# Optimization experiments

Measured on AMD Instinct MI355X. Metric: run time of the kernel, lower is better.

The kernel has to match this reference:

```python
import jax, jax.numpy as jnp
import numpy as np

B, T, V, E, H = 64, 512, 8192, 1024, 2048


def setup_inputs() -> dict:
    key = jax.random.key(0)
    k = jax.random.split(key, 8)
    idx = jax.random.randint(k[0], (B, T), 0, V)
    targets = jax.random.randint(k[1], (B, T), 0, V)
    s = 0.02
    W_E = jax.random.normal(k[2], (V, E), jnp.float32) * s
    start = jnp.zeros((1, H), jnp.float32)
    W_xh = jax.random.normal(k[3], (E + H, H), jnp.float32) * s  # Linear(E+H -> H)
    b_xh = jnp.zeros((H,), jnp.float32)
    W_head = jax.random.normal(k[4], (H, V), jnp.float32) * s
    b_head = jnp.zeros((V,), jnp.float32)
    return {"idx": idx, "targets": targets, "W_E": W_E, "start": start,
            "W_xh": W_xh, "b_xh": b_xh, "W_head": W_head, "b_head": b_head}


def reference(idx, targets, W_E, start, W_xh, b_xh, W_head, b_head):
    b, t = idx.shape
    emb = W_E[idx]  # [B, T, E]
    # split concat-linear: cat([x,h]) @ W_xh == x @ Wx + h @ Wh (same math)
    Wx, Wh = W_xh[:E], W_xh[E:]
    xproj = jnp.einsum('bte,eh->bth', emb, Wx) + b_xh  # precompute input part

    def step(h_prev, xp_t):
        h_t = jnp.tanh(xp_t + h_prev @ Wh)
        return h_t, h_t

    h0 = jnp.broadcast_to(start, (b, H))
    _, hs = jax.lax.scan(step, h0, jnp.swapaxes(xproj, 0, 1))  # [T, B, H]
    hidden = jnp.swapaxes(hs, 0, 1)  # [B, T, H]
    logits = jnp.einsum('bth,hv->btv', hidden, W_head) + b_head

    # cross entropy with ignore_index=-1
    logp = jax.nn.log_softmax(logits, axis=-1)
    mask = targets != -1
    tsafe = jnp.where(mask, targets, 0)
    nll = -jnp.take_along_axis(logp, tsafe[..., None], axis=-1)[..., 0]
    loss = jnp.sum(nll * mask) / jnp.maximum(jnp.sum(mask), 1)
    return logits, loss
```

## Files before the change

### kernel.cpp

```cpp
#include <hip/hip_runtime.h>
#include <hip/hip_bf16.h>
#include <math.h>
#include <stdint.h>

#define Bb 64
#define Tt 512
#define Vv 8192
#define Ee 1024
#define Hh 2048

typedef unsigned short u16;
typedef unsigned long long u64;
typedef __attribute__((ext_vector_type(8))) short bf16x8;
typedef __attribute__((ext_vector_type(8))) _Float16 f16x8;
typedef __attribute__((ext_vector_type(4))) float f32x4;

__device__ __forceinline__ u16 f2b(float f) {
  unsigned u = __float_as_uint(f);
  u += 0x7FFF + ((u >> 16) & 1);
  return (u16)(u >> 16);
}
__device__ __forceinline__ float b2f(u16 h) {
  return __uint_as_float(((unsigned)h) << 16);
}
__device__ __forceinline__ u16 f2h_bits(float f) {
  union { _Float16 h; u16 u; } c;
  c.h = (_Float16)f;
  return c.u;
}
__device__ __forceinline__ u64 pack4(u16 a, u16 b, u16 c, u16 d) {
  return (u64)a | ((u64)b << 16) | ((u64)c << 32) | ((u64)d << 48);
}

__device__ __forceinline__ void gload16f(f16x8& dst, const void* addr) {
  asm volatile("global_load_dwordx4 %0, %1, off sc1"
               : "=v"(dst) : "v"(addr) : "memory");
}

__device__ __forceinline__ void gll16(const u16* g, u16* l) {
  __builtin_amdgcn_global_load_lds((__attribute__((address_space(1))) void*)g,
                                   (__attribute__((address_space(3))) void*)l, 16, 0, 0);
}

__device__ __forceinline__ float wave_max(float v) {
  #pragma unroll
  for (int d = 32; d; d >>= 1) v = fmaxf(v, __shfl_xor(v, d, 64));
  return v;
}
__device__ __forceinline__ float wave_sum(float v) {
  #pragma unroll
  for (int d = 32; d; d >>= 1) v += __shfl_xor(v, d, 64);
  return v;
}


__global__ __launch_bounds__(256)
void embed_cast(const float* __restrict__ WE, const int* __restrict__ idx,
                u16* __restrict__ emb2) {
  const int m = blockIdx.x;
  const int row = idx[m];
  const float4 v = ((const float4*)(WE + (size_t)row * Ee))[threadIdx.x];
  ushort4 hi, lo;
  hi.x = f2b(v.x); lo.x = f2b(v.x - b2f(hi.x));
  hi.y = f2b(v.y); lo.y = f2b(v.y - b2f(hi.y));
  hi.z = f2b(v.z); lo.z = f2b(v.z - b2f(hi.z));
  hi.w = f2b(v.w); lo.w = f2b(v.w - b2f(hi.w));
  u16* d = emb2 + (size_t)m * 2048;
  ((ushort4*)d)[threadIdx.x] = hi;
  ((ushort4*)(d + Ee))[threadIdx.x] = lo;
}

__global__ __launch_bounds__(256)
void transpose_cast(const float* __restrict__ src, u16* __restrict__ dst,
                    int R, int C, int dup) {
  __shared__ float tile[32][33];
  const int bi = blockIdx.x;
  const int bj = blockIdx.y;
  const int tid = threadIdx.x;
  const int r  = tid >> 3;
  const int c4 = (tid & 7) * 4;
  float4 v = *(const float4*)(src + (size_t)(bj * 32 + r) * C + bi * 32 + c4);
  tile[r][c4 + 0] = v.x; tile[r][c4 + 1] = v.y;
  tile[r][c4 + 2] = v.z; tile[r][c4 + 3] = v.w;
  __syncthreads();
  const int RL = R << dup;
  ushort4 o;
  o.x = f2b(tile[c4 + 0][r]); o.y = f2b(tile[c4 + 1][r]);
  o.z = f2b(tile[c4 + 2][r]); o.w = f2b(tile[c4 + 3][r]);
  u16* d = dst + (size_t)(bi * 32 + r) * RL + bj * 32 + c4;
  *(ushort4*)d = o;
  if (dup) *(ushort4*)(d + R) = o;
}

__global__ __launch_bounds__(256)
void transpose_cast_f16(const float* __restrict__ src, u16* __restrict__ dst,
                        int R, int C) {
  __shared__ float tile[32][33];
  const int bi = blockIdx.x;
  const int bj = blockIdx.y;
  const int tid = threadIdx.x;
  const int r  = tid >> 3;
  const int c4 = (tid & 7) * 4;
  float4 v = *(const float4*)(src + (size_t)(bj * 32 + r) * C + bi * 32 + c4);
  tile[r][c4 + 0] = v.x; tile[r][c4 + 1] = v.y;
  tile[r][c4 + 2] = v.z; tile[r][c4 + 3] = v.w;
  __syncthreads();
  ushort4 o;
  o.x = f2h_bits(tile[c4 + 0][r]); o.y = f2h_bits(tile[c4 + 1][r]);
  o.z = f2h_bits(tile[c4 + 2][r]); o.w = f2h_bits(tile[c4 + 3][r]);
  *(ushort4*)(dst + (size_t)(bi * 32 + r) * R + bj * 32 + c4) = o;
}

__global__ __launch_bounds__(256)
void h0_init(const float* __restrict__ start, u16* __restrict__ hbuf) {
  const int b = blockIdx.x;
  #pragma unroll
  for (int j = 0; j < 8; ++j) {
    int n = threadIdx.x * 8 + j;
    hbuf[(size_t)b * 2048 + n] = f2h_bits(start[n]);
  }
}

template <int MODE>
__global__ __launch_bounds__(256, 2)
void gemm_bt(const u16* __restrict__ A, const u16* __restrict__ Bt,
             const float* __restrict__ bias, void* __restrict__ outp,
             float* __restrict__ pm, float* __restrict__ ps,
             int M, int N, int K) {
  __shared__ u16 ldsA[128 * 32];
  __shared__ u16 ldsB[128 * 32];
  __shared__ float sm_[2][2][64];
  __shared__ float ss_[2][2][64];
  const int tid = threadIdx.x;
  const int lane = tid & 63;
  const int w = tid >> 6;
  const int wr = w >> 1, wc = w & 1;

  const int nwg = gridDim.x * gridDim.y;
  const int lin = blockIdx.y * gridDim.x + blockIdx.x;
  const int swz = (lin & 7) * (nwg >> 3) + (lin >> 3);
  const int bm = swz % gridDim.x;
  const int bn = swz / gridDim.x;

  const int srow = w * 32 + (lane >> 2);
  const int scol = (lane & 3) * 8;
  const u16* a0 = A + (size_t)(bm * 128 + srow) * K + scol;
  const u16* b0 = Bt + (size_t)(bn * 128 + srow) * K + scol;
  u16* lA0 = ldsA + w * 1024;
  u16* lA1 = ldsA + w * 1024 + 512;
  u16* lB0 = ldsB + w * 1024;
  u16* lB1 = ldsB + w * 1024 + 512;

  f32x4 acc[4][4];
  #pragma unroll
  for (int m = 0; m < 4; ++m)
    #pragma unroll
    for (int n = 0; n < 4; ++n)
      acc[m][n] = (f32x4){0.f, 0.f, 0.f, 0.f};

  const int nk = K >> 5;
  for (int kt = 0; kt < nk; ++kt) {
    __syncthreads();
    const u16* ak = a0 + kt * 32;
    const u16* bk = b0 + kt * 32;
    gll16(ak, lA0);
    gll16(ak + 16 * (size_t)K, lA1);
    gll16(bk, lB0);
    gll16(bk + 16 * (size_t)K, lB1);
    __syncthreads();
    bf16x8 af[4], bfr[4];
    #pragma unroll
    for (int i = 0; i < 4; ++i) {
      af[i]  = *(const bf16x8*)&ldsA[(wr * 64 + i * 16 + (lane & 15)) * 32 + (lane >> 4) * 8];
      bfr[i] = *(const bf16x8*)&ldsB[(wc * 64 + i * 16 + (lane & 15)) * 32 + (lane >> 4) * 8];
    }
    #pragma unroll
    for (int m = 0; m < 4; ++m)
      #pragma unroll
      for (int n = 0; n < 4; ++n)
        acc[m][n] = __builtin_amdgcn_mfma_f32_16x16x32_bf16(af[m], bfr[n], acc[m][n], 0, 0, 0);
  }

  const int r0 = bm * 128 + wr * 64 + (lane >> 4) * 4;
  const int c0 = bn * 128 + wc * 64 + (lane & 15);

  if (MODE == 0) {
    float bv[4];
    #pragma unroll
    for (int n = 0; n < 4; ++n) bv[n] = bias[c0 + n * 16];
    #pragma unroll
    for (int m = 0; m < 4; ++m) {
      #pragma unroll
      for (int q = 0; q < 4; ++q) {
        const int row = r0 + m * 16 + q;
        float v[4];
        float mx = -1e30f;
        #pragma unroll
        for (int n = 0; n < 4; ++n) {
          v[n] = acc[m][n][q] + bv[n];
          ((float*)outp)[(size_t)row * N + c0 + n * 16] = v[n];
          mx = fmaxf(mx, v[n]);
        }
        #pragma unroll
        for (int d = 1; d < 16; d <<= 1) mx = fmaxf(mx, __shfl_xor(mx, d, 64));
        float se = 0.f;
        #pragma unroll
        for (int n = 0; n < 4; ++n) se += expf(v[n] - mx);
        #pragma unroll
        for (int d = 1; d < 16; d <<= 1) se += __shfl_xor(se, d, 64);
        if ((lane & 15) == 0) {
          const int rl = m * 16 + (lane >> 4) * 4 + q;
          sm_[wc][wr][rl] = mx;
          ss_[wc][wr][rl] = se;
        }
      }
    }
    __syncthreads();
    if (w < 2) {
      float m0 = sm_[0][w][lane], m1 = sm_[1][w][lane];
      float s0 = ss_[0][w][lane], s1 = ss_[1][w][lane];
      float Mx = fmaxf(m0, m1);
      float S = s0 * expf(m0 - Mx) + s1 * expf(m1 - Mx);
      const int row = bm * 128 + w * 64 + lane;
      pm[(size_t)row * 64 + bn] = Mx;
      ps[(size_t)row * 64 + bn] = S;
    }
  } else {
    #pragma unroll
    for (int n = 0; n < 4; ++n) {
      const int col = c0 + n * 16;
      const float bv = bias[col];
      #pragma unroll
      for (int m = 0; m < 4; ++m) {
        #pragma unroll
        for (int q = 0; q < 4; ++q) {
          const int row = r0 + m * 16 + q;
          float v = acc[m][n][q] + bv;
          const int b = row >> 9, t = row & 511;
          ((u16*)outp)[((size_t)t * Bb + b) * N + col] = f2b(v);
        }
      }
    }
  }
}

__global__ __launch_bounds__(512, 2)
void rnn_scan(const u16* __restrict__ WhT, const u16* __restrict__ xp,
              u16* __restrict__ hbuf, u16* __restrict__ hidden,
              unsigned* __restrict__ sync) {
  __shared__ u16 whi[65536];
  __shared__ float red[4096];

  const int bid = blockIdx.x;
  const int g = bid >> 6;
  const int colg = bid & 63;
  const int rowbase = g * 16;
  const int col0 = colg * 32;
  const int tid = threadIdx.x;
  const int lane = tid & 63;
  const int w = tid >> 6;

  for (int i = tid; i < 8192; i += 512) {
    const int ch = i & 3;
    const int cl = (i >> 2) & 15;
    const int kt = (i >> 6) & 63;
    const int c2 = (i >> 12) & 1;
    bf16x8 v = *(const bf16x8*)(WhT + (size_t)(col0 + c2 * 16 + cl) * 2048 + kt * 32 + ch * 8);
    *(bf16x8*)&whi[(size_t)(c2 * 64 + kt) * 512 + ch * 128 + cl * 8] = v;
  }
  __syncthreads();

  unsigned* cnt = sync + g * 64;
  bool dead = false;

  const int hrow = rowbase + (lane & 15);

  ushort4 xv = {0, 0, 0, 0};
  if (w < 2)
    xv = *(const ushort4*)(xp + (size_t)hrow * 2048 + col0 + w * 16 + (lane >> 4) * 4);

  for (int t = 0; t < Tt; ++t) {
    const u16* hp = hbuf + (size_t)(t & 1) * (64 * 2048);
    u16*       hn = hbuf + (size_t)((t + 1) & 1) * (64 * 2048);

    f16x8 qh[8];
    const u16* hb = hp + (size_t)hrow * 2048 + (lane >> 4) * 8;
    #pragma unroll
    for (int kt = 0; kt < 8; ++kt)
      gload16f(qh[kt], hb + (w * 8 + kt) * 32);
    asm volatile("s_waitcnt vmcnt(0)" ::: "memory");
    __builtin_amdgcn_sched_barrier(0);

    f32x4 a0 = (f32x4){0.f, 0.f, 0.f, 0.f};
    f32x4 a1 = (f32x4){0.f, 0.f, 0.f, 0.f};
    #pragma unroll
    for (int kt = 0; kt < 8; ++kt) {
      const int ktG = w * 8 + kt;
      f16x8 w0 = *(const f16x8*)&whi[(size_t)(0 * 64 + ktG) * 512 + (lane >> 4) * 128 + (lane & 15) * 8];
      f16x8 w1 = *(const f16x8*)&whi[(size_t)(1 * 64 + ktG) * 512 + (lane >> 4) * 128 + (lane & 15) * 8];
      a0 = __builtin_amdgcn_mfma_f32_16x16x32_f16(w0, qh[kt], a0, 0, 0, 0);
      a1 = __builtin_amdgcn_mfma_f32_16x16x32_f16(w1, qh[kt], a1, 0, 0, 0);
    }

    *(f32x4*)&red[(w) * 256 + lane * 4]     = a0;
    *(f32x4*)&red[(8 + w) * 256 + lane * 4] = a1;
    __syncthreads();

    if (w < 2) {
      f32x4 ac = (f32x4){0.f, 0.f, 0.f, 0.f};
      #pragma unroll
      for (int j = 0; j < 8; ++j)
        ac += *(const f32x4*)&red[(w * 8 + j) * 256 + lane * 4];
      const int cl0 = (lane >> 4) * 4;
      u16 hf[4], hbv[4];
      #pragma unroll
      for (int qq = 0; qq < 4; ++qq) {
        float v = tanhf(ac[qq] + b2f(((const u16*)&xv)[qq]));
        hf[qq]  = f2h_bits(v);
        hbv[qq] = f2b(v);
      }
      u64 ph = pack4(hf[0], hf[1], hf[2], hf[3]);
      u64 pb = pack4(hbv[0], hbv[1], hbv[2], hbv[3]);
      u16* hd = hn + (size_t)hrow * 2048 + col0 + w * 16 + cl0;
      __hip_atomic_store((u64*)hd, ph, __ATOMIC_RELAXED, __HIP_MEMORY_SCOPE_AGENT);
      *(u64*)(hidden + ((size_t)hrow * Tt + t) * Hh + col0 + w * 16 + cl0) = pb;
    }

    __syncthreads();
    if (w < 2 && t + 1 < Tt)
      xv = *(const ushort4*)(xp + ((size_t)(t + 1) * Bb + hrow) * 2048 + col0 + w * 16 + (lane >> 4) * 4);
    if (tid == 0) {
      unsigned old = __hip_atomic_fetch_add(cnt, 1u, __ATOMIC_RELAXED, __HIP_MEMORY_SCOPE_AGENT);
      if (old != (unsigned)(t * 64 + 63) && !dead) {
        unsigned polls = 0;
        while (__hip_atomic_load(cnt, __ATOMIC_RELAXED, __HIP_MEMORY_SCOPE_AGENT)
               < (unsigned)((t + 1) * 64)) {
          if (++polls > 4000000u) { dead = true; break; }
        }
      }
    }
    __syncthreads();
  }
}


__global__ __launch_bounds__(256)
void nll_from_partials(const float* __restrict__ pm, const float* __restrict__ ps,
                       const float* __restrict__ logits, const int* __restrict__ tgt,
                       float* __restrict__ nll) {
  const int r = blockIdx.x * 4 + (threadIdx.x >> 6);
  const int lane = threadIdx.x & 63;
  float m = pm[(size_t)r * 64 + lane];
  float s = ps[(size_t)r * 64 + lane];
  float M = wave_max(m);
  float S = wave_sum(s * expf(m - M));
  if (lane == 0) {
    const int tg = tgt[r];
    float o = 0.f;
    if (tg != -1) o = M + logf(S) - logits[(size_t)r * Vv + tg];
    nll[r] = o;
  }
}

__global__ __launch_bounds__(256)
void loss_reduce(const float* __restrict__ nll, const int* __restrict__ tgt,
                 float* __restrict__ out) {
  const int tid = threadIdx.x;
  float s = 0.f, c = 0.f;
  for (int i = tid; i < Bb * Tt; i += 256) {
    s += nll[i];
    c += (tgt[i] != -1) ? 1.f : 0.f;
  }
  s = wave_sum(s);
  c = wave_sum(c);
  __shared__ float as_[4], ac_[4];
  const int w = tid >> 6;
  if ((tid & 63) == 0) { as_[w] = s; ac_[w] = c; }
  __syncthreads();
  if (tid == 0) {
    float S = as_[0] + as_[1] + as_[2] + as_[3];
    float C = ac_[0] + ac_[1] + ac_[2] + ac_[3];
    out[0] = S / fmaxf(C, 1.f);
  }
}


extern "C" void kernel_launch(void* const* d_in, const int* in_sizes, int n_in,
                              void* d_out, int out_size, void* d_ws, size_t ws_size,
                              hipStream_t stream) {
  const int*   idx    = (const int*)d_in[0];
  const int*   tgt    = (const int*)d_in[1];
  const float* W_E    = (const float*)d_in[2];
  const float* start  = (const float*)d_in[3];
  const float* W_xh   = (const float*)d_in[4];
  const float* b_xh   = (const float*)d_in[5];
  const float* W_head = (const float*)d_in[6];
  const float* b_head = (const float*)d_in[7];

  char* ws = (char*)d_ws;
  u16*      emb2   = (u16*)(ws);
  u16*      hidden = (u16*)(ws);
  u16*      xproj  = (u16*)(ws + (size_t)128 * 1024 * 1024);
  float*    pm     = (float*)(ws + (size_t)128 * 1024 * 1024);
  float*    ps     = (float*)(ws + (size_t)136 * 1024 * 1024);
  u16*      WheadT = (u16*)(ws + (size_t)256 * 1024 * 1024);
  u16*      WhT    = (u16*)(ws + (size_t)288 * 1024 * 1024);
  u16*      WxT2   = (u16*)(ws + (size_t)304 * 1024 * 1024);
  u16*      hbuf   = (u16*)(ws + (size_t)312 * 1024 * 1024);
  float*    nll    = (float*)(ws + (size_t)313 * 1024 * 1024);
  unsigned* sync   = (unsigned*)(ws + (size_t)313 * 1024 * 1024 + 128 * 1024);

  embed_cast<<<Bb * Tt, 256, 0, stream>>>(W_E, idx, emb2);
  transpose_cast<<<dim3(Hh / 32, Ee / 32), 256, 0, stream>>>(W_xh, WxT2, Ee, Hh, 1);
  transpose_cast_f16<<<dim3(Hh / 32, Hh / 32), 256, 0, stream>>>(W_xh + (size_t)Ee * Hh, WhT, Hh, Hh);
  transpose_cast<<<dim3(Vv / 32, Hh / 32), 256, 0, stream>>>(W_head, WheadT, Hh, Vv, 0);
  h0_init<<<Bb, 256, 0, stream>>>(start, hbuf);
  hipMemsetAsync(sync, 0, 1024, stream);

  gemm_bt<1><<<dim3(256, 16), 256, 0, stream>>>(emb2, WxT2, b_xh, xproj, nullptr, nullptr,
                                                Bb * Tt, Hh, 2048);

  rnn_scan<<<256, 512, 0, stream>>>(WhT, xproj, hbuf, hidden, sync);

  gemm_bt<0><<<dim3(256, 64), 256, 0, stream>>>(hidden, WheadT, b_head, d_out, pm, ps,
                                                Bb * Tt, Vv, 2048);

  nll_from_partials<<<Bb * Tt / 4, 256, 0, stream>>>(pm, ps, (const float*)d_out, tgt, nll);
  loss_reduce<<<1, 256, 0, stream>>>(nll, tgt, (float*)d_out + ((size_t)out_size - 1));
}
```

Baseline: 4.554 ms.

## Replace 128x128 GEMM with double-buffered 256x256 tile GEMM using swizzled LDS

Replaces the simple 128x128 tile GEMM, which synchronised on every K=32 step, with a 512-thread 256x256 tile kernel. It uses K=64 steps, double-buffered LDS staging interleaved with MFMA phases, an XOR-swizzled LDS layout to avoid bank conflicts, and s_setprio around the MFMA bursts. Both the input projection and the head projection now use it, and the softmax partials shrink from 64 to 32 per row, so the NLL kernel is updated to match. The aim is to hide global-load latency and raise data reuse per tile. In exchange it uses 128KB of LDS with one block per CU and needs a larger register footprint.

```diff
diff --git a/kernel.cpp b/kernel.cpp
--- a/kernel.cpp
+++ b/kernel.cpp
@@ -37,7 +37,7 @@
                : "=v"(dst) : "v"(addr) : "memory");
 }
 
-__device__ __forceinline__ void gll16(const u16* g, u16* l) {
+__device__ __forceinline__ void gll16(const u16* g, const u16* l) {
   __builtin_amdgcn_global_load_lds((__attribute__((address_space(1))) void*)g,
                                    (__attribute__((address_space(3))) void*)l, 16, 0, 0);
 }
@@ -121,124 +121,175 @@
   }
 }
 
+#define A0BASE 0
+#define A1BASE 16384
+#define B0BASE 32768
+#define B1BASE 49152
+#define MM(a, b, c) __builtin_amdgcn_mfma_f32_16x16x32_bf16(a, b, c, 0, 0, 0)
+
+#define DSA(AB, MH, KS, I) \
+  (*(const bf16x8*)&lds[(AB) + (wm * 128 + ((MH) * 4 + (I)) * 16 + l15) * 64 + (((KS) * 32 + l16 * 8) ^ axr)])
+#define DSB(BB, KS, J) \
+  (*(const bf16x8*)&lds[(BB) + (wn * 64 + (J) * 16 + l15) * 64 + (((KS) * 32 + l16 * 8) ^ axr)])
+
+#define PHASE(ABUF, BBUF, MH, KS, RB, STG)                                   \
+  {                                                                          \
+    bf16x8 a0_ = DSA(ABUF, MH, KS, 0), a1_ = DSA(ABUF, MH, KS, 1),           \
+           a2_ = DSA(ABUF, MH, KS, 2), a3_ = DSA(ABUF, MH, KS, 3);           \
+    if (RB) {                                                                \
+      b0_ = DSB(BBUF, KS, 0); b1_ = DSB(BBUF, KS, 1);                        \
+      b2_ = DSB(BBUF, KS, 2); b3_ = DSB(BBUF, KS, 3);                        \
+    }                                                                        \
+    STG;                                                                     \
+    asm volatile("s_waitcnt vmcnt(4)" ::: "memory");                         \
+    __builtin_amdgcn_s_barrier();                                            \
+    asm volatile("s_waitcnt lgkmcnt(0)" ::: "memory");                       \
+    __builtin_amdgcn_sched_barrier(0);                                       \
+    __builtin_amdgcn_s_setprio(1);                                           \
+    acc[(MH)*4+0][0] = MM(a0_, b0_, acc[(MH)*4+0][0]);                       \
+    acc[(MH)*4+0][1] = MM(a0_, b1_, acc[(MH)*4+0][1]);                       \
+    acc[(MH)*4+0][2] = MM(a0_, b2_, acc[(MH)*4+0][2]);                       \
+    acc[(MH)*4+0][3] = MM(a0_, b3_, acc[(MH)*4+0][3]);                       \
+    acc[(MH)*4+1][0] = MM(a1_, b0_, acc[(MH)*4+1][0]);                       \
+    acc[(MH)*4+1][1] = MM(a1_, b1_, acc[(MH)*4+1][1]);                       \
+    acc[(MH)*4+1][2] = MM(a1_, b2_, acc[(MH)*4+1][2]);                       \
+    acc[(MH)*4+1][3] = MM(a1_, b3_, acc[(MH)*4+1][3]);                       \
+    acc[(MH)*4+2][0] = MM(a2_, b0_, acc[(MH)*4+2][0]);                       \
+    acc[(MH)*4+2][1] = MM(a2_, b1_, acc[(MH)*4+2][1]);                       \
+    acc[(MH)*4+2][2] = MM(a2_, b2_, acc[(MH)*4+2][2]);                       \
+    acc[(MH)*4+2][3] = MM(a2_, b3_, acc[(MH)*4+2][3]);                       \
+    acc[(MH)*4+3][0] = MM(a3_, b0_, acc[(MH)*4+3][0]);                       \
+    acc[(MH)*4+3][1] = MM(a3_, b1_, acc[(MH)*4+3][1]);                       \
+    acc[(MH)*4+3][2] = MM(a3_, b2_, acc[(MH)*4+3][2]);                       \
+    acc[(MH)*4+3][3] = MM(a3_, b3_, acc[(MH)*4+3][3]);                       \
+    __builtin_amdgcn_s_setprio(0);                                           \
+    __builtin_amdgcn_s_barrier();                                            \
+  }
+
 template <int MODE>
-__global__ __launch_bounds__(256, 2)
-void gemm_bt(const u16* __restrict__ A, const u16* __restrict__ Bt,
+__global__ __launch_bounds__(512)
+void gemm256(const u16* __restrict__ A, const u16* __restrict__ Bt,
              const float* __restrict__ bias, void* __restrict__ outp,
              float* __restrict__ pm, float* __restrict__ ps,
              int M, int N, int K) {
-  __shared__ u16 ldsA[128 * 32];
-  __shared__ u16 ldsB[128 * 32];
-  __shared__ float sm_[2][2][64];
-  __shared__ float ss_[2][2][64];
+  __shared__ u16 lds[65536];
+
   const int tid = threadIdx.x;
   const int lane = tid & 63;
   const int w = tid >> 6;
-  const int wr = w >> 1, wc = w & 1;
+  const int wm = w >> 2;
+  const int wn = w & 3;
+  const int l15 = lane & 15, l16 = lane >> 4;
+  const int axr = (l15 & 7) << 3;
 
   const int nwg = gridDim.x * gridDim.y;
   const int lin = blockIdx.y * gridDim.x + blockIdx.x;
   const int swz = (lin & 7) * (nwg >> 3) + (lin >> 3);
   const int bm = swz % gridDim.x;
   const int bn = swz / gridDim.x;
-
-  const int srow = w * 32 + (lane >> 2);
-  const int scol = (lane & 3) * 8;
-  const u16* a0 = A + (size_t)(bm * 128 + srow) * K + scol;
-  const u16* b0 = Bt + (size_t)(bn * 128 + srow) * K + scol;
-  u16* lA0 = ldsA + w * 1024;
-  u16* lA1 = ldsA + w * 1024 + 512;
-  u16* lB0 = ldsB + w * 1024;
-  u16* lB1 = ldsB + w * 1024 + 512;
-
-  f32x4 acc[4][4];
+  const int bm256 = bm * 256, bn256 = bn * 256;
+
+  const int sj8 = lane >> 3;
+  const int scb = (((lane & 7) * 16) ^ ((sj8 & 7) << 4)) >> 1;
+
+  #define STAGE(src, r0, kt, lbase)                                          \
+    {                                                                        \
+      _Pragma("unroll")                                                      \
+      for (int j_ = 0; j_ < 2; ++j_) {                                       \
+        const int chunk_ = w * 2 + j_;                                       \
+        gll16(src + (size_t)((r0) + chunk_ * 8 + sj8) * K + (kt) * 64 + scb, \
+              &lds[(lbase) + chunk_ * 512]);                                 \
+      }                                                                      \
+    }
+
+  f32x4 acc[8][4];
   #pragma unroll
-  for (int m = 0; m < 4; ++m)
+  for (int m = 0; m < 8; ++m)
     #pragma unroll
     for (int n = 0; n < 4; ++n)
       acc[m][n] = (f32x4){0.f, 0.f, 0.f, 0.f};
-
-  const int nk = K >> 5;
-  for (int kt = 0; kt < nk; ++kt) {
-    __syncthreads();
-    const u16* ak = a0 + kt * 32;
-    const u16* bk = b0 + kt * 32;
-    gll16(ak, lA0);
-    gll16(ak + 16 * (size_t)K, lA1);
-    gll16(bk, lB0);
-    gll16(bk + 16 * (size_t)K, lB1);
-    __syncthreads();
-    bf16x8 af[4], bfr[4];
+  bf16x8 b0_, b1_, b2_, b3_;
+
+  STAGE(Bt, bn256,       0, B0BASE);
+  STAGE(Bt, bn256 + 128, 0, B0BASE + 8192);
+  STAGE(A,  bm256,       0, A0BASE);
+  STAGE(A,  bm256 + 128, 0, A0BASE + 8192);
+  STAGE(A,  bm256,       1, A1BASE);
+  asm volatile("s_waitcnt vmcnt(0)" ::: "memory");
+  __builtin_amdgcn_s_barrier();
+
+  const int NG = K >> 7;
+  for (int g = 0; g < NG; ++g) {
+    const int t1 = 2 * g + 1, t2 = 2 * g + 2, t3 = 2 * g + 3;
+    const bool more = (g + 1 < NG);
+    PHASE(A0BASE, B0BASE, 0, 0, true,  STAGE(Bt, bn256,       t1, B1BASE))
+    PHASE(A0BASE, B0BASE, 1, 0, false, STAGE(Bt, bn256 + 128, t1, B1BASE + 8192))
+    PHASE(A0BASE, B0BASE, 0, 1, true,  STAGE(A,  bm256 + 128, t1, A1BASE + 8192))
+    PHASE(A0BASE, B0BASE, 1, 1, false, if (more) STAGE(Bt, bn256,       t2, B0BASE))
+    PHASE(A1BASE, B1BASE, 0, 0, true,  if (more) STAGE(Bt, bn256 + 128, t2, B0BASE + 8192))
+    PHASE(A1BASE, B1BASE, 1, 0, false, if (more) STAGE(A,  bm256,       t2, A0BASE))
+    PHASE(A1BASE, B1BASE, 0, 1, true,  if (more) STAGE(A,  bm256 + 128, t2, A0BASE + 8192))
+    PHASE(A1BASE, B1BASE, 1, 1, false, if (more) STAGE(A,  bm256,       t3, A1BASE))
+  }
+
+  const int c0 = bn256 + wn * 64 + l15;
+  float bv[4];
+  #pragma unroll
+  for (int j = 0; j < 4; ++j) bv[j] = bias[c0 + j * 16];
+
+  if (MODE == 0) {
+    float* scr = (float*)lds;
+    float* outf = (float*)outp;
     #pragma unroll
-    for (int i = 0; i < 4; ++i) {
-      af[i]  = *(const bf16x8*)&ldsA[(wr * 64 + i * 16 + (lane & 15)) * 32 + (lane >> 4) * 8];
-      bfr[i] = *(const bf16x8*)&ldsB[(wc * 64 + i * 16 + (lane & 15)) * 32 + (lane >> 4) * 8];
-    }
-    #pragma unroll
-    for (int m = 0; m < 4; ++m)
-      #pragma unroll
-      for (int n = 0; n < 4; ++n)
-        acc[m][n] = __builtin_amdgcn_mfma_f32_16x16x32_bf16(af[m], bfr[n], acc[m][n], 0, 0, 0);
-  }
-
-  const int r0 = bm * 128 + wr * 64 + (lane >> 4) * 4;
-  const int c0 = bn * 128 + wc * 64 + (lane & 15);
-
-  if (MODE == 0) {
-    float bv[4];
-    #pragma unroll
-    for (int n = 0; n < 4; ++n) bv[n] = bias[c0 + n * 16];
-    #pragma unroll
-    for (int m = 0; m < 4; ++m) {
+    for (int fm = 0; fm < 8; ++fm) {
       #pragma unroll
       for (int q = 0; q < 4; ++q) {
-        const int row = r0 + m * 16 + q;
-        float v[4];
-        float mx = -1e30f;
-        #pragma unroll
-        for (int n = 0; n < 4; ++n) {
-          v[n] = acc[m][n][q] + bv[n];
-          ((float*)outp)[(size_t)row * N + c0 + n * 16] = v[n];
-          mx = fmaxf(mx, v[n]);
-        }
+        const int rl = wm * 128 + fm * 16 + l16 * 4 + q;
+        const int row = bm256 + rl;
+        float v0 = acc[fm][0][q] + bv[0];
+        float v1 = acc[fm][1][q] + bv[1];
+        float v2 = acc[fm][2][q] + bv[2];
+        float v3 = acc[fm][3][q] + bv[3];
+        outf[(size_t)row * N + c0]      = v0;
+        outf[(size_t)row * N + c0 + 16] = v1;
+        outf[(size_t)row * N + c0 + 32] = v2;
+        outf[(size_t)row * N + c0 + 48] = v3;
+        float mx = fmaxf(fmaxf(v0, v1), fmaxf(v2, v3));
         #pragma unroll
         for (int d = 1; d < 16; d <<= 1) mx = fmaxf(mx, __shfl_xor(mx, d, 64));
-        float se = 0.f;
-        #pragma unroll
-        for (int n = 0; n < 4; ++n) se += expf(v[n] - mx);
+        float se = expf(v0 - mx) + expf(v1 - mx) + expf(v2 - mx) + expf(v3 - mx);
         #pragma unroll
         for (int d = 1; d < 16; d <<= 1) se += __shfl_xor(se, d, 64);
-        if ((lane & 15) == 0) {
-          const int rl = m * 16 + (lane >> 4) * 4 + q;
-          sm_[wc][wr][rl] = mx;
-          ss_[wc][wr][rl] = se;
+        if (l15 == 0) {
+          scr[wn * 256 + rl] = mx;
+          scr[1024 + wn * 256 + rl] = se;
         }
       }
     }
     __syncthreads();
-    if (w < 2) {
-      float m0 = sm_[0][w][lane], m1 = sm_[1][w][lane];
-      float s0 = ss_[0][w][lane], s1 = ss_[1][w][lane];
-      float Mx = fmaxf(m0, m1);
-      float S = s0 * expf(m0 - Mx) + s1 * expf(m1 - Mx);
-      const int row = bm * 128 + w * 64 + lane;
-      pm[(size_t)row * 64 + bn] = Mx;
-      ps[(size_t)row * 64 + bn] = S;
+    if (lane < 32) {
+      const int rl = w * 32 + lane;
+      float m0 = scr[rl], m1 = scr[256 + rl], m2 = scr[512 + rl], m3 = scr[768 + rl];
+      float Mx = fmaxf(fmaxf(m0, m1), fmaxf(m2, m3));
+      float S = scr[1024 + rl] * expf(m0 - Mx) + scr[1280 + rl] * expf(m1 - Mx)
+              + scr[1536 + rl] * expf(m2 - Mx) + scr[1792 + rl] * expf(m3 - Mx);
+      const int row = bm256 + rl;
+      pm[(size_t)row * 32 + bn] = Mx;
+      ps[(size_t)row * 32 + bn] = S;
     }
   } else {
+    u16* outh = (u16*)outp;
     #pragma unroll
-    for (int n = 0; n < 4; ++n) {
-      const int col = c0 + n * 16;
-      const float bv = bias[col];
+    for (int fm = 0; fm < 8; ++fm) {
       #pragma unroll
-      for (int m = 0; m < 4; ++m) {
-        #pragma unroll
-        for (int q = 0; q < 4; ++q) {
-          const int row = r0 + m * 16 + q;
-          float v = acc[m][n][q] + bv;
-          const int b = row >> 9, t = row & 511;
-          ((u16*)outp)[((size_t)t * Bb + b) * N + col] = f2b(v);
-        }
+      for (int q = 0; q < 4; ++q) {
+        const int row = bm256 + wm * 128 + fm * 16 + l16 * 4 + q;
+        const int b = row >> 9, t = row & 511;
+        u16* dst = outh + ((size_t)t * Bb + b) * N + c0;
+        dst[0]  = f2b(acc[fm][0][q] + bv[0]);
+        dst[16] = f2b(acc[fm][1][q] + bv[1]);
+        dst[32] = f2b(acc[fm][2][q] + bv[2]);
+        dst[48] = f2b(acc[fm][3][q] + bv[3]);
       }
     }
   }
@@ -272,7 +323,6 @@
 
   unsigned* cnt = sync + g * 64;
   bool dead = false;
-
   const int hrow = rowbase + (lane & 15);
 
   ushort4 xv = {0, 0, 0, 0};
@@ -350,8 +400,8 @@
                        float* __restrict__ nll) {
   const int r = blockIdx.x * 4 + (threadIdx.x >> 6);
   const int lane = threadIdx.x & 63;
-  float m = pm[(size_t)r * 64 + lane];
-  float s = ps[(size_t)r * 64 + lane];
+  float m = (lane < 32) ? pm[(size_t)r * 32 + lane] : -1e30f;
+  float s = (lane < 32) ? ps[(size_t)r * 32 + lane] : 0.f;
   float M = wave_max(m);
   float S = wave_sum(s * expf(m - M));
   if (lane == 0) {
@@ -417,12 +467,12 @@
   h0_init<<<Bb, 256, 0, stream>>>(start, hbuf);
   hipMemsetAsync(sync, 0, 1024, stream);
 
-  gemm_bt<1><<<dim3(256, 16), 256, 0, stream>>>(emb2, WxT2, b_xh, xproj, nullptr, nullptr,
-                                                Bb * Tt, Hh, 2048);
+  gemm256<1><<<dim3(128, 8), 512, 0, stream>>>(emb2, WxT2, b_xh, xproj, nullptr, nullptr,
+                                               Bb * Tt, Hh, 2048);
 
   rnn_scan<<<256, 512, 0, stream>>>(WhT, xproj, hbuf, hidden, sync);
 
-  gemm_bt<0><<<dim3(256, 64), 256, 0, stream>>>(hidden, WheadT, b_head, d_out, pm, ps,
+  gemm256<0><<<dim3(128, 32), 512, 0, stream>>>(hidden, WheadT, b_head, d_out, pm, ps,
                                                 Bb * Tt, Vv, 2048);
 
   nll_from_partials<<<Bb * Tt / 4, 256, 0, stream>>>(pm, ps, (const float*)d_out, tgt, nll);
```

Result: slower. 4.749 ms (+4.3%).
